# Kernel tuning notes

Hardware: AMD Instinct MI355X
Metric: run time of the kernel (lower is better)

Reference implementation:

```python
import jax, jax.numpy as jnp
import numpy as np

M = 8      # num_modules
H = 128    # hidden_size per module
IN = 512   # input_size
MH = M * H

def _block_mask():
    # mask[mi*H:(mi+1)*H, mi*H:] = 1 (module mi reads modules >= mi)
    m = np.zeros((MH, MH), dtype=np.float32)
    for mi in range(M):
        m[mi*H:(mi+1)*H, mi*H:] = 1.0
    return jnp.asarray(m)

def _active_sizes(T):
    # number of active modules at step t: t=0 -> M, else min(M, trailing_zeros(t)+1)
    sizes = []
    for t in range(T):
        ma = 0
        while t % (2 ** ma) == 0 and ma < M:
            ma += 1
        sizes.append(ma * H)
    return jnp.asarray(np.array(sizes, dtype=np.int32))

def setup_inputs() -> dict:
    key = jax.random.key(0)
    k1, k2, k3, k4 = jax.random.split(key, 4)
    T, B = 256, 128
    scale = 1.0 / np.sqrt(MH)
    x = jax.random.normal(k1, (T, B, IN), dtype=jnp.float32)
    h_prev = jnp.zeros((B, MH), dtype=jnp.float32)
    Wxh = jax.random.normal(k2, (MH, IN), dtype=jnp.float32) * scale
    Whh = jax.random.normal(k3, (MH, MH), dtype=jnp.float32) * scale
    bh = jax.random.normal(k4, (MH,), dtype=jnp.float32) * scale
    return {"x": x, "h_prev": h_prev, "Wxh": Wxh, "Whh": Whh, "bh": bh}

def reference(x, h_prev, Wxh, Whh, bh):
    T = x.shape[0]
    mask = _block_mask()
    Whh_m = Whh * mask  # clockwork block-triangular mask, reapplied as in torch
    thresholds = _active_sizes(T)          # [T] active hidden width per step
    idx = jnp.arange(MH)

    # Precompute input projections for all timesteps: [T, B, MH]
    xW = jnp.einsum('tbi,hi->tbh', x, Wxh)

    def step(h, inp):
        xw_t, thr = inp
        # full-width update; rows < thr equal the torch sliced-matmul result
        h_full = h @ Whh_m.T + xw_t + bh
        h_new = jnp.where(idx < thr, h_full, h)
        return h_new, h_new

    h_last, out = jax.lax.scan(step, h_prev, (xW, thresholds))
    return (out, h_last)
```

## Files before the change

kernel.cpp:

```cpp
#include <hip/hip_runtime.h>
#include <hip/hip_bf16.h>


#define TT 256
#define BB 128
#define INW 512
#define HH 128
#define MHW 1024

typedef __bf16 bf16x8 __attribute__((ext_vector_type(8)));
typedef __bf16 bf16x4 __attribute__((ext_vector_type(4)));
typedef float f32x4 __attribute__((ext_vector_type(4)));

__constant__ unsigned int c_hmod_off[8] = {
    0u, 4194304u, 6291456u, 7340032u, 7864320u, 8126464u, 8257536u, 8323072u};

__device__ __forceinline__ int active_thr(int t) {
    int ma = (t == 0) ? 8 : min(__ffs(t), 8);
    return ma * HH;
}

__device__ __forceinline__ unsigned short f2bf(float f) {
    union { float f; unsigned int u; } v{f};
    unsigned int r = v.u + 0x7FFFu + ((v.u >> 16) & 1u);
    return (unsigned short)(r >> 16);
}
__device__ __forceinline__ unsigned int pack2(float lo, float hi) {
    return (unsigned int)f2bf(lo) | ((unsigned int)f2bf(hi) << 16);
}
__device__ __forceinline__ float bf2f(unsigned short u) {
    union { unsigned int i; float f; } v;
    v.i = ((unsigned int)u) << 16;
    return v.f;
}

__device__ __forceinline__ void gld_lds16(const void* g, char* l) {
    __builtin_amdgcn_global_load_lds(
        (const __attribute__((address_space(1))) void*)g,
        (__attribute__((address_space(3))) void*)l, 16, 0, 0);
}

__device__ __forceinline__ bf16x8 frag_ld(const char* tile, int row, int ks, int lane) {
    int off = (row * 128 + ks * 64 + (lane >> 4) * 16) ^ ((row & 7) << 4);
    return *reinterpret_cast<const bf16x8*>(tile + off);
}

__device__ __forceinline__ bf16x8 frag_ld_f32(const char* tile, int row, int ks, int g) {
    int off = ((row << 8) + ks * 128 + g * 32) ^ ((row & 7) << 4);
    f32x4 a = *reinterpret_cast<const f32x4*>(tile + off);
    f32x4 b = *reinterpret_cast<const f32x4*>(tile + (off ^ 16));
    bf16x8 u;
    u[0] = (__bf16)a[0]; u[1] = (__bf16)a[1]; u[2] = (__bf16)a[2]; u[3] = (__bf16)a[3];
    u[4] = (__bf16)b[0]; u[5] = (__bf16)b[1]; u[6] = (__bf16)b[2]; u[7] = (__bf16)b[3];
    return u;
}

__global__ __launch_bounds__(256) void k_xw(const float* __restrict__ x,
                                            const float* __restrict__ Wxh,
                                            const float* __restrict__ bh,
                                            float* __restrict__ xwb) {
    __shared__ char ldsW[2][32768];
    __shared__ char ldsX[2][16384];
    int id = blockIdx.x >> 1, half = blockIdx.x & 1;
    int rt = 0, rem = id;
    while (rem >= (256 >> rt)) { rem -= 256 >> rt; ++rt; }
    int t = rem << rt;

    int tid = threadIdx.x, lane = tid & 63, wid = tid >> 6;
    int l15 = lane & 15, g = lane >> 4;
    int wr = (wid >> 1) * 64, wc = (wid & 1) * 32;

    const float* gW[8];
    const float* gX[4];
    {
        int kb = (lane & 15) * 16;
#pragma unroll
        for (int i = 0; i < 8; ++i) {
            int row = i * 16 + wid * 4 + (lane >> 4);
            int kf = (kb ^ ((row & 7) << 4)) >> 2;
            gW[i] = Wxh + (size_t)(rt * 128 + row) * INW + kf;
        }
#pragma unroll
        for (int i = 0; i < 4; ++i) {
            int row = i * 16 + wid * 4 + (lane >> 4);
            int kf = (kb ^ ((row & 7) << 4)) >> 2;
            gX[i] = x + ((size_t)t * BB + half * 64 + row) * INW + kf;
        }
    }
#pragma unroll
    for (int i = 0; i < 8; ++i)
        gld_lds16(gW[i], &ldsW[0][0] + i * 4096 + wid * 1024);
#pragma unroll
    for (int i = 0; i < 4; ++i)
        gld_lds16(gX[i], &ldsX[0][0] + i * 4096 + wid * 1024);

    f32x4 acc[4][2] = {};
    for (int c = 0; c < 8; ++c) {
        int cur = c & 1;
        __syncthreads();
        if (c < 7) {
#pragma unroll
            for (int i = 0; i < 8; ++i)
                gld_lds16(gW[i] + (c + 1) * 64,
                          &ldsW[cur ^ 1][0] + i * 4096 + wid * 1024);
#pragma unroll
            for (int i = 0; i < 4; ++i)
                gld_lds16(gX[i] + (c + 1) * 64,
                          &ldsX[cur ^ 1][0] + i * 4096 + wid * 1024);
        }
#pragma unroll
        for (int ks = 0; ks < 2; ++ks) {
            bf16x8 fa[4], fb[2];
#pragma unroll
            for (int i = 0; i < 4; ++i)
                fa[i] = frag_ld_f32(&ldsW[cur][0], wr + i * 16 + l15, ks, g);
#pragma unroll
            for (int j = 0; j < 2; ++j)
                fb[j] = frag_ld_f32(&ldsX[cur][0], wc + j * 16 + l15, ks, g);
#pragma unroll
            for (int i = 0; i < 4; ++i)
#pragma unroll
                for (int j = 0; j < 2; ++j)
                    acc[i][j] = __builtin_amdgcn_mfma_f32_16x16x32_bf16(
                        fa[i], fb[j], acc[i][j], 0, 0, 0);
        }
    }
#pragma unroll
    for (int i = 0; i < 4; ++i) {
        int rbase = rt * 128 + wr + i * 16 + g * 4;
        float4 bias = *reinterpret_cast<const float4*>(&bh[rbase]);
#pragma unroll
        for (int j = 0; j < 2; ++j) {
            int b = half * 64 + wc + j * 16 + l15;
            float4 v = make_float4(acc[i][j][0] + bias.x, acc[i][j][1] + bias.y,
                                   acc[i][j][2] + bias.z, acc[i][j][3] + bias.w);
            *reinterpret_cast<float4*>(
                &xwb[(size_t)(t * BB + b) * MHW + rbase]) = v;
        }
    }
}

__global__ __launch_bounds__(256) void k_u(const float* __restrict__ Whh,
                                           const float* __restrict__ hprev,
                                           const unsigned short* __restrict__ hmod,
                                           float* __restrict__ xwb, int mi) {
    __shared__ char lds[131072];
    char* ldsA0 = lds;
    char* ldsA1 = lds + 32768;
    char* ldsH0 = lds + 65536;
    char* ldsH1 = lds + 98304;
    int k = blockIdx.x;
    int t = k << mi;
    int tid = threadIdx.x, lane = tid & 63, wid = tid >> 6;
    int l15 = lane & 15, g = lane >> 4;
    int wr = (wid >> 1) * 64, wc = (wid & 1) * 64;
    int ntile = 2 * (7 - mi);

    const float* gA[8];
    {
        int kb = l15 * 16;
#pragma unroll
        for (int i = 0; i < 8; ++i) {
            int row = i * 16 + wid * 4 + g;
            int kf = (kb ^ ((row & 7) << 4)) >> 2;
            gA[i] = Whh + (size_t)(mi * HH + row) * MHW + kf;
        }
    }
    f32x4 acc[4][4] = {};

    if (k == 0) {
        const float* gH[8];
        {
            int kb = l15 * 16;
#pragma unroll
            for (int i = 0; i < 8; ++i) {
                int row = i * 16 + wid * 4 + g;
                int kf = (kb ^ ((row & 7) << 4)) >> 2;
                gH[i] = hprev + (size_t)row * MHW + kf;
            }
        }
        auto stage = [&](int tt, char* dA, char* dH) {
            int j = mi + 1 + (tt >> 1), c0 = (tt & 1) * 64;
            int off = j * HH + c0;
#pragma unroll
            for (int i = 0; i < 8; ++i)
                gld_lds16(gA[i] + off, dA + i * 4096 + wid * 1024);
#pragma unroll
            for (int i = 0; i < 8; ++i)
                gld_lds16(gH[i] + off, dH + i * 4096 + wid * 1024);
        };
        stage(0, ldsA0, ldsH0);
        for (int tt = 0; tt < ntile; ++tt) {
            int cur = tt & 1;
            __syncthreads();
            if (tt + 1 < ntile)
                stage(tt + 1, cur ? ldsA0 : ldsA1, cur ? ldsH0 : ldsH1);
            const char* sA = cur ? ldsA1 : ldsA0;
            const char* sH = cur ? ldsH1 : ldsH0;
#pragma unroll
            for (int ks = 0; ks < 2; ++ks) {
                bf16x8 fa[4], fb[4];
#pragma unroll
                for (int i = 0; i < 4; ++i) {
                    fa[i] = frag_ld_f32(sA, wr + i * 16 + l15, ks, g);
                    fb[i] = frag_ld_f32(sH, wc + i * 16 + l15, ks, g);
                }
#pragma unroll
                for (int i = 0; i < 4; ++i)
#pragma unroll
                    for (int jj = 0; jj < 4; ++jj)
                        acc[i][jj] = __builtin_amdgcn_mfma_f32_16x16x32_bf16(
                            fa[i], fb[jj], acc[i][jj], 0, 0, 0);
            }
        }
    } else {
        size_t hoff[4];
        {
            int cb = ((lane & 7) * 16) ^ ((lane >> 3) << 4);
#pragma unroll
            for (int p = 0; p < 4; ++p) {
                int row = p * 32 + wid * 8 + (lane >> 3);
                hoff[p] = (size_t)row * HH + (cb >> 1);
            }
        }
        auto stage = [&](int tt, char* dA, char* dH) {
            int j = mi + 1 + (tt >> 1), c0 = (tt & 1) * 64;
            int offA = j * HH + c0;
#pragma unroll
            for (int i = 0; i < 8; ++i)
                gld_lds16(gA[i] + offA, dA + i * 4096 + wid * 1024);
            const unsigned short* hb =
                hmod + c_hmod_off[j] + (size_t)((t - 1) >> j) * BB * HH + c0;
#pragma unroll
            for (int p = 0; p < 4; ++p)
                gld_lds16(hb + hoff[p], dH + p * 4096 + wid * 1024);
        };
        stage(0, ldsA0, ldsH0);
        for (int tt = 0; tt < ntile; ++tt) {
            int cur = tt & 1;
            __syncthreads();
            if (tt + 1 < ntile)
                stage(tt + 1, cur ? ldsA0 : ldsA1, cur ? ldsH0 : ldsH1);
            const char* sA = cur ? ldsA1 : ldsA0;
            const char* sH = cur ? ldsH1 : ldsH0;
#pragma unroll
            for (int ks = 0; ks < 2; ++ks) {
                bf16x8 fa[4], fb[4];
#pragma unroll
                for (int i = 0; i < 4; ++i) {
                    fa[i] = frag_ld_f32(sA, wr + i * 16 + l15, ks, g);
                    fb[i] = frag_ld(sH, wc + i * 16 + l15, ks, lane);
                }
#pragma unroll
                for (int i = 0; i < 4; ++i)
#pragma unroll
                    for (int jj = 0; jj < 4; ++jj)
                        acc[i][jj] = __builtin_amdgcn_mfma_f32_16x16x32_bf16(
                            fa[i], fb[jj], acc[i][jj], 0, 0, 0);
            }
        }
    }
#pragma unroll
    for (int i = 0; i < 4; ++i) {
        int rbase = wr + i * 16 + g * 4;
#pragma unroll
        for (int j = 0; j < 4; ++j) {
            int b = wc + j * 16 + l15;
            float4* p = reinterpret_cast<float4*>(
                &xwb[(size_t)(t * BB + b) * MHW + mi * HH + rbase]);
            float4 v = *p;
            v.x += acc[i][j][0]; v.y += acc[i][j][1];
            v.z += acc[i][j][2]; v.w += acc[i][j][3];
            *p = v;
        }
    }
}

#define SYNC_LDS()                                              \
    do {                                                        \
        asm volatile("s_waitcnt lgkmcnt(0)" ::: "memory");      \
        __builtin_amdgcn_sched_barrier(0);                      \
        __builtin_amdgcn_s_barrier();                           \
        __builtin_amdgcn_sched_barrier(0);                      \
    } while (0)
#define SYNC_VM24()                                             \
    do {                                                        \
        asm volatile("s_waitcnt vmcnt(24)" ::: "memory");       \
        __builtin_amdgcn_sched_barrier(0);                      \
        __builtin_amdgcn_s_barrier();                           \
        __builtin_amdgcn_sched_barrier(0);                      \
    } while (0)

__global__ __launch_bounds__(256) void k_phase(const float* __restrict__ Whh,
                                               const float* __restrict__ hprev,
                                               const float* __restrict__ xwb,
                                               unsigned short* __restrict__ hmod,
                                               int mi) {
    int b0 = blockIdx.x * 16;
    int tid = threadIdx.x, lane = tid & 63, wid = tid >> 6;
    int l15 = lane & 15, g = lane >> 4;
    __shared__ char sH[2][4096];
    __shared__ char sU[8][8192];
    int Tm = TT >> mi;

    if (wid < 2) {
        bf16x8 Af[4][4];
        {
            const float* Ab = Whh + (size_t)(mi * HH) * MHW + mi * HH;
#pragma unroll
            for (int mm = 0; mm < 4; ++mm) {
                const float* row = Ab + (size_t)(64 * wid + mm * 16 + l15) * MHW;
#pragma unroll
                for (int kf = 0; kf < 4; ++kf) {
                    float4 v0 = *reinterpret_cast<const float4*>(row + kf * 32 + g * 8);
                    float4 v1 = *reinterpret_cast<const float4*>(row + kf * 32 + g * 8 + 4);
                    bf16x8 u;
                    u[0] = (__bf16)v0.x; u[1] = (__bf16)v0.y;
                    u[2] = (__bf16)v0.z; u[3] = (__bf16)v0.w;
                    u[4] = (__bf16)v1.x; u[5] = (__bf16)v1.y;
                    u[6] = (__bf16)v1.z; u[7] = (__bf16)v1.w;
                    Af[mm][kf] = u;
                }
            }
        }
#pragma unroll
        for (int p = 0; p < 2; ++p) {
            int tt = tid + p * 128;
            int b = tt >> 4, r8 = (tt & 15) * 8;
            const float* hp = hprev + (size_t)(b0 + b) * MHW + mi * HH + r8;
            float4 v0 = *reinterpret_cast<const float4*>(hp);
            float4 v1 = *reinterpret_cast<const float4*>(hp + 4);
            uint4 pk;
            pk.x = pack2(v0.x, v0.y); pk.y = pack2(v0.z, v0.w);
            pk.z = pack2(v1.x, v1.y); pk.w = pack2(v1.z, v1.w);
            int off = (b * 256 + r8 * 2) ^ ((b & 7) << 4);
            *reinterpret_cast<uint4*>(&sH[0][0] + off) = pk;
        }
        int roff[4], woff[4], uoff[4];
#pragma unroll
        for (int kf = 0; kf < 4; ++kf)
            roff[kf] = (l15 * 256 + kf * 64 + g * 16) ^ ((l15 & 7) << 4);
#pragma unroll
        for (int mm = 0; mm < 4; ++mm) {
            woff[mm] = (l15 * 256 + (64 * wid + mm * 16 + g * 4) * 2) ^ ((l15 & 7) << 4);
            uoff[mm] = (16 * wid + 4 * mm + g) * 256 + l15 * 16;
        }
        SYNC_LDS();

        for (int K = 0; K < Tm; ++K) {
            int cur = K & 1;
            const char* ub = &sU[K & 7][0];
            f32x4 acc[4], acc2[4];
#pragma unroll
            for (int mm = 0; mm < 4; ++mm) {
                acc[mm] = *reinterpret_cast<const f32x4*>(ub + uoff[mm]);
                acc2[mm] = (f32x4){0.f, 0.f, 0.f, 0.f};
            }
            bf16x8 Bf[4];
#pragma unroll
            for (int kf = 0; kf < 4; ++kf)
                Bf[kf] = *reinterpret_cast<const bf16x8*>(&sH[cur][0] + roff[kf]);
#pragma unroll
            for (int mm = 0; mm < 4; ++mm) {
                acc[mm] = __builtin_amdgcn_mfma_f32_16x16x32_bf16(
                    Af[mm][0], Bf[0], acc[mm], 0, 0, 0);
                acc2[mm] = __builtin_amdgcn_mfma_f32_16x16x32_bf16(
                    Af[mm][2], Bf[2], acc2[mm], 0, 0, 0);
                acc[mm] = __builtin_amdgcn_mfma_f32_16x16x32_bf16(
                    Af[mm][1], Bf[1], acc[mm], 0, 0, 0);
                acc2[mm] = __builtin_amdgcn_mfma_f32_16x16x32_bf16(
                    Af[mm][3], Bf[3], acc2[mm], 0, 0, 0);
            }
#pragma unroll
            for (int mm = 0; mm < 4; ++mm) {
                acc[mm] += acc2[mm];
                bf16x4 pk;
                pk[0] = (__bf16)acc[mm][0]; pk[1] = (__bf16)acc[mm][1];
                pk[2] = (__bf16)acc[mm][2]; pk[3] = (__bf16)acc[mm][3];
                *reinterpret_cast<bf16x4*>(&sH[cur ^ 1][0] + woff[mm]) = pk;
            }
            SYNC_LDS();
        }
    } else if (wid == 2) {
        const float* ubase = xwb + (size_t)(b0 + l15) * MHW + mi * HH + g * 4;
#pragma unroll
        for (int q = 0; q < 4; ++q) {
            int t = min(q, Tm - 1) << mi;
            const float* pt = ubase + (size_t)t * BB * MHW;
#pragma unroll
            for (int p = 0; p < 8; ++p)
                gld_lds16(pt + p * 16, &sU[q][0] + p * 1024);
        }
        SYNC_VM24();
        for (int K = 0; K < Tm; ++K) {
            int t = min(K + 4, Tm - 1) << mi;
            int slot = (K + 4) & 7;
            const float* pt = ubase + (size_t)t * BB * MHW;
#pragma unroll
            for (int p = 0; p < 8; ++p)
                gld_lds16(pt + p * 16, &sU[slot][0] + p * 1024);
            SYNC_VM24();
        }
        asm volatile("s_waitcnt vmcnt(0)" ::: "memory");
    } else {
        int bq = lane >> 2;
        int rr = (lane & 3) * 32;
        unsigned short* hm =
            hmod + c_hmod_off[mi] + (size_t)(b0 + bq) * HH + rr;
        int soff[4];
#pragma unroll
        for (int c = 0; c < 4; ++c)
            soff[c] = (bq * 256 + (rr + c * 8) * 2) ^ ((bq & 7) << 4);
        SYNC_LDS();
        for (int K = 0; K < Tm; ++K) {
            if (K >= 1) {
                uint4 h[4];
#pragma unroll
                for (int c = 0; c < 4; ++c)
                    h[c] = *reinterpret_cast<const uint4*>(&sH[K & 1][0] + soff[c]);
                unsigned short* dst = hm + (size_t)(K - 1) * BB * HH;
#pragma unroll
                for (int c = 0; c < 4; ++c)
                    *reinterpret_cast<uint4*>(dst + c * 8) = h[c];
            }
            SYNC_LDS();
        }
        {
            uint4 h[4];
#pragma unroll
            for (int c = 0; c < 4; ++c)
                h[c] = *reinterpret_cast<const uint4*>(&sH[Tm & 1][0] + soff[c]);
            unsigned short* dst = hm + (size_t)(Tm - 1) * BB * HH;
#pragma unroll
            for (int c = 0; c < 4; ++c)
                *reinterpret_cast<uint4*>(dst + c * 8) = h[c];
        }
    }
}

__global__ __launch_bounds__(256) void k_out(const unsigned short* __restrict__ hmod,
                                             float* __restrict__ out) {
    int b = blockIdx.x, t = blockIdx.y;
    int tid = threadIdx.x;
    int i = tid * 4;
    int j = i >> 7;
    int k = t >> j;
    ushort4 h = *reinterpret_cast<const ushort4*>(
        &hmod[c_hmod_off[j] + ((size_t)k * BB + b) * HH + (i & 127)]);
    float4 v = make_float4(bf2f(h.x), bf2f(h.y), bf2f(h.z), bf2f(h.w));
    *reinterpret_cast<float4*>(&out[((size_t)t * BB + b) * MHW + i]) = v;
    if (t == TT - 1) {
        *reinterpret_cast<float4*>(
            &out[(size_t)TT * BB * MHW + (size_t)b * MHW + i]) = v;
    }
}

extern "C" void kernel_launch(void* const* d_in, const int* in_sizes, int n_in,
                              void* d_out, int out_size, void* d_ws, size_t ws_size,
                              hipStream_t stream) {
    const float* x = (const float*)d_in[0];
    const float* hprev = (const float*)d_in[1];
    const float* Wxh = (const float*)d_in[2];
    const float* Whh = (const float*)d_in[3];
    const float* bh = (const float*)d_in[4];
    float* out = (float*)d_out;

    float* xwb = out;
    unsigned short* hmod = (unsigned short*)d_ws;

    k_xw<<<dim3(1020), 256, 0, stream>>>(x, Wxh, bh, xwb);

    for (int mi = 7; mi >= 0; --mi) {
        if (mi < 7)
            k_u<<<dim3(TT >> mi), 256, 0, stream>>>(Whh, hprev, hmod, xwb, mi);
        k_phase<<<8, 256, 0, stream>>>(Whh, hprev, xwb, hmod, mi);
    }

    k_out<<<dim3(128, 256), 256, 0, stream>>>(hmod, out);
}
```

Measured before the change: 404.1 us.

## Parallelize serial recurrence for fast modules via matrix-power chunked scan

For modules 0 and 1 (the longest sequential chains), the recurrence is split into chunks of 8 steps. Powers of the diagonal Whh block are precomputed (k_pow), and in-chunk partial sums are built in parallel (k_s). Only chunk boundaries run serially, using the 8th power (k_comb), and the intermediate states are then expanded in parallel (k_exp). This shortens the serial dependency chain by about 8x in exchange for extra matmul work and more kernel launches. Repeated bf16 rounding of the matrix powers may also add numerical error.

```diff
diff --git a/kernel.cpp b/kernel.cpp
--- a/kernel.cpp
+++ b/kernel.cpp
@@ -15,11 +15,6 @@
 __constant__ unsigned int c_hmod_off[8] = {
     0u, 4194304u, 6291456u, 7340032u, 7864320u, 8126464u, 8257536u, 8323072u};
 
-__device__ __forceinline__ int active_thr(int t) {
-    int ma = (t == 0) ? 8 : min(__ffs(t), 8);
-    return ma * HH;
-}
-
 __device__ __forceinline__ unsigned short f2bf(float f) {
     union { float f; unsigned int u; } v{f};
     unsigned int r = v.u + 0x7FFFu + ((v.u >> 16) & 1u);
@@ -40,11 +35,33 @@
         (__attribute__((address_space(3))) void*)l, 16, 0, 0);
 }
 
+__device__ __forceinline__ void stage_load(float4 (&v)[8],
+                                           const float* __restrict__ src,
+                                           int stride, int tid) {
+    int k4 = (tid & 15) * 4;
+    int r0 = tid >> 4;
+#pragma unroll
+    for (int p = 0; p < 8; ++p)
+        v[p] = *reinterpret_cast<const float4*>(src + (size_t)(p * 16 + r0) * stride + k4);
+}
+__device__ __forceinline__ void stage_write(char* dst, const float4 (&v)[8], int tid) {
+    int k8 = (tid & 15) * 8;
+    int r0 = tid >> 4;
+#pragma unroll
+    for (int p = 0; p < 8; ++p) {
+        int row = p * 16 + r0;
+        ushort4 b;
+        b.x = f2bf(v[p].x); b.y = f2bf(v[p].y);
+        b.z = f2bf(v[p].z); b.w = f2bf(v[p].w);
+        int off = (row * 128 + k8) ^ ((row & 7) << 4);
+        *reinterpret_cast<ushort4*>(dst + off) = b;
+    }
+}
+
 __device__ __forceinline__ bf16x8 frag_ld(const char* tile, int row, int ks, int lane) {
     int off = (row * 128 + ks * 64 + (lane >> 4) * 16) ^ ((row & 7) << 4);
     return *reinterpret_cast<const bf16x8*>(tile + off);
 }
-
 __device__ __forceinline__ bf16x8 frag_ld_f32(const char* tile, int row, int ks, int g) {
     int off = ((row << 8) + ks * 128 + g * 32) ^ ((row & 7) << 4);
     f32x4 a = *reinterpret_cast<const f32x4*>(tile + off);
@@ -53,6 +70,26 @@
     u[0] = (__bf16)a[0]; u[1] = (__bf16)a[1]; u[2] = (__bf16)a[2]; u[3] = (__bf16)a[3];
     u[4] = (__bf16)b[0]; u[5] = (__bf16)b[1]; u[6] = (__bf16)b[2]; u[7] = (__bf16)b[3];
     return u;
+}
+
+__device__ __forceinline__ void mfma_tile(const char* sA, const char* sB,
+                                          f32x4 (&acc)[4][4], int lane,
+                                          int wr, int wc) {
+#pragma unroll
+    for (int ks = 0; ks < 2; ++ks) {
+        bf16x8 fa[4], fb[4];
+#pragma unroll
+        for (int i = 0; i < 4; ++i) {
+            fa[i] = frag_ld(sA, wr + i * 16 + (lane & 15), ks, lane);
+            fb[i] = frag_ld(sB, wc + i * 16 + (lane & 15), ks, lane);
+        }
+#pragma unroll
+        for (int i = 0; i < 4; ++i)
+#pragma unroll
+            for (int j = 0; j < 4; ++j)
+                acc[i][j] = __builtin_amdgcn_mfma_f32_16x16x32_bf16(
+                    fa[i], fb[j], acc[i][j], 0, 0, 0);
+    }
 }
 
 __global__ __launch_bounds__(256) void k_xw(const float* __restrict__ x,
@@ -137,6 +174,70 @@
             *reinterpret_cast<float4*>(
                 &xwb[(size_t)(t * BB + b) * MHW + rbase]) = v;
         }
+    }
+}
+
+__global__ __launch_bounds__(256) void k_pow(const float* __restrict__ Whh,
+                                             float* __restrict__ P) {
+    int mi = blockIdx.x;
+    __shared__ char X[2][16384];
+    __shared__ char Bt[2][16384];
+    int tid = threadIdx.x, lane = tid & 63, wid = tid >> 6;
+    int l15 = lane & 15, g = lane >> 4;
+    int wr = (wid >> 1) * 64, wc = (wid & 1) * 64;
+    const float* Ab = Whh + (size_t)(mi * HH) * MHW + mi * HH;
+    float* Pm = P + (size_t)mi * 8 * 16384;
+
+#pragma unroll
+    for (int ck = 0; ck < 2; ++ck) {
+        float4 vA[8];
+        stage_load(vA, Ab + ck * 64, MHW, tid);
+        stage_write(&X[ck][0], vA, tid);
+        int k4 = (tid & 15) * 4;
+        int r0 = tid >> 4;
+#pragma unroll
+        for (int p = 0; p < 8; ++p) {
+            int row = p * 16 + r0;
+            ushort4 b;
+            b.x = f2bf(Ab[(size_t)(ck * 64 + k4 + 0) * MHW + row]);
+            b.y = f2bf(Ab[(size_t)(ck * 64 + k4 + 1) * MHW + row]);
+            b.z = f2bf(Ab[(size_t)(ck * 64 + k4 + 2) * MHW + row]);
+            b.w = f2bf(Ab[(size_t)(ck * 64 + k4 + 3) * MHW + row]);
+            int off = (row * 128 + k4 * 2) ^ ((row & 7) << 4);
+            *reinterpret_cast<ushort4*>(&Bt[ck][0] + off) = b;
+        }
+    }
+    for (int idx = tid * 4; idx < 16384; idx += 1024) {
+        int r = idx >> 7, cq = idx & 127;
+        *reinterpret_cast<float4*>(&Pm[idx]) =
+            *reinterpret_cast<const float4*>(&Ab[(size_t)r * MHW + cq]);
+    }
+    __syncthreads();
+
+    for (int q = 1; q < 8; ++q) {
+        f32x4 acc[4][4] = {};
+        mfma_tile(&X[0][0], &Bt[0][0], acc, lane, wr, wc);
+        mfma_tile(&X[1][0], &Bt[1][0], acc, lane, wr, wc);
+        __syncthreads();
+        float* Pq = Pm + (size_t)q * 16384;
+#pragma unroll
+        for (int i = 0; i < 4; ++i) {
+            int r0 = wr + i * 16 + g * 4;
+#pragma unroll
+            for (int jq = 0; jq < 4; ++jq) {
+                int c = wc + jq * 16 + l15;
+#pragma unroll
+                for (int rr = 0; rr < 4; ++rr) {
+                    float v = acc[i][jq][rr];
+                    Pq[(size_t)(r0 + rr) * 128 + c] = v;
+                    int ck = c >> 6;
+                    int off = (((r0 + rr) * 128) + (c & 63) * 2) ^
+                              (((r0 + rr) & 7) << 4);
+                    *reinterpret_cast<__bf16*>(&X[ck][0] + off) = (__bf16)v;
+                }
+            }
+        }
+        __syncthreads();
     }
 }
 
@@ -276,6 +377,87 @@
     }
 }
 
+__global__ __launch_bounds__(256) void k_s(const float* __restrict__ P,
+                                           float* __restrict__ xwb, int mi) {
+    __shared__ char lds[131072];
+    char* ldsA0 = lds;
+    char* ldsA1 = lds + 32768;
+    char* ldsH0 = lds + 65536;
+    char* ldsH1 = lds + 98304;
+    int c = blockIdx.x, i = blockIdx.y;
+    int tid = threadIdx.x, lane = tid & 63, wid = tid >> 6;
+    int l15 = lane & 15, g = lane >> 4;
+    int wr = (wid >> 1) * 64, wc = (wid & 1) * 64;
+    int mcol = mi * HH, scol = (mi + 1) * HH;
+    int ntile = 2 * i;
+    f32x4 acc[4][4] = {};
+
+    if (ntile > 0) {
+        const float* gA[8];
+        const float* gH[8];
+        {
+            int kb = l15 * 16;
+#pragma unroll
+            for (int i_ = 0; i_ < 8; ++i_) {
+                int row = i_ * 16 + wid * 4 + g;
+                int kf = (kb ^ ((row & 7) << 4)) >> 2;
+                gA[i_] = P + (size_t)row * 128 + kf;
+                gH[i_] = xwb + (size_t)row * MHW + mcol + kf;
+            }
+        }
+        auto stage = [&](int tt, char* dA, char* dH) {
+            int p = tt >> 1, c0 = (tt & 1) * 64;
+            size_t offA = (size_t)(mi * 8 + (i - 1 - p)) * 16384 + c0;
+            size_t offH = (size_t)((8 * c + p) << mi) * BB * MHW + c0;
+#pragma unroll
+            for (int i_ = 0; i_ < 8; ++i_)
+                gld_lds16(gA[i_] + offA, dA + i_ * 4096 + wid * 1024);
+#pragma unroll
+            for (int i_ = 0; i_ < 8; ++i_)
+                gld_lds16(gH[i_] + offH, dH + i_ * 4096 + wid * 1024);
+        };
+        stage(0, ldsA0, ldsH0);
+        for (int tt = 0; tt < ntile; ++tt) {
+            int cur = tt & 1;
+            __syncthreads();
+            if (tt + 1 < ntile)
+                stage(tt + 1, cur ? ldsA0 : ldsA1, cur ? ldsH0 : ldsH1);
+            const char* sA = cur ? ldsA1 : ldsA0;
+            const char* sH = cur ? ldsH1 : ldsH0;
+#pragma unroll
+            for (int ks = 0; ks < 2; ++ks) {
+                bf16x8 fa[4], fb[4];
+#pragma unroll
+                for (int i_ = 0; i_ < 4; ++i_) {
+                    fa[i_] = frag_ld_f32(sA, wr + i_ * 16 + l15, ks, g);
+                    fb[i_] = frag_ld_f32(sH, wc + i_ * 16 + l15, ks, g);
+                }
+#pragma unroll
+                for (int i_ = 0; i_ < 4; ++i_)
+#pragma unroll
+                    for (int jj = 0; jj < 4; ++jj)
+                        acc[i_][jj] = __builtin_amdgcn_mfma_f32_16x16x32_bf16(
+                            fa[i_], fb[jj], acc[i_][jj], 0, 0, 0);
+            }
+        }
+    }
+    int tI = (8 * c + i) << mi;
+#pragma unroll
+    for (int i_ = 0; i_ < 4; ++i_) {
+        int rbase = wr + i_ * 16 + g * 4;
+#pragma unroll
+        for (int j = 0; j < 4; ++j) {
+            int b = wc + j * 16 + l15;
+            float4 u4 = *reinterpret_cast<const float4*>(
+                &xwb[(size_t)(tI * BB + b) * MHW + mcol + rbase]);
+            float4 v = make_float4(acc[i_][j][0] + u4.x, acc[i_][j][1] + u4.y,
+                                   acc[i_][j][2] + u4.z, acc[i_][j][3] + u4.w);
+            *reinterpret_cast<float4*>(
+                &xwb[(size_t)(tI * BB + b) * MHW + scol + rbase]) = v;
+        }
+    }
+}
+
 #define SYNC_LDS()                                              \
     do {                                                        \
         asm volatile("s_waitcnt lgkmcnt(0)" ::: "memory");      \
@@ -291,6 +473,268 @@
         __builtin_amdgcn_sched_barrier(0);                      \
     } while (0)
 
+__global__ __launch_bounds__(256) void k_comb(const float* __restrict__ P,
+                                              const float* __restrict__ hprev,
+                                              const float* __restrict__ xwb,
+                                              unsigned short* __restrict__ hmod,
+                                              int mi) {
+    int b0 = blockIdx.x * 16;
+    int tid = threadIdx.x, lane = tid & 63, wid = tid >> 6;
+    int l15 = lane & 15, g = lane >> 4;
+    __shared__ char sH[2][4096];
+    __shared__ char sU[8][8192];
+    int C = (TT >> mi) >> 3;
+    int scol = (mi + 1) * HH;
+    const float* P8 = P + (size_t)(mi * 8 + 7) * 16384;
+
+    if (wid < 2) {
+        bf16x8 Af[4][4];
+        {
+#pragma unroll
+            for (int mm = 0; mm < 4; ++mm) {
+                const float* row = P8 + (size_t)(64 * wid + mm * 16 + l15) * 128;
+#pragma unroll
+                for (int kf = 0; kf < 4; ++kf) {
+                    float4 v0 = *reinterpret_cast<const float4*>(row + kf * 32 + g * 8);
+                    float4 v1 = *reinterpret_cast<const float4*>(row + kf * 32 + g * 8 + 4);
+                    bf16x8 u;
+                    u[0] = (__bf16)v0.x; u[1] = (__bf16)v0.y;
+                    u[2] = (__bf16)v0.z; u[3] = (__bf16)v0.w;
+                    u[4] = (__bf16)v1.x; u[5] = (__bf16)v1.y;
+                    u[6] = (__bf16)v1.z; u[7] = (__bf16)v1.w;
+                    Af[mm][kf] = u;
+                }
+            }
+        }
+#pragma unroll
+        for (int p = 0; p < 2; ++p) {
+            int tt = tid + p * 128;
+            int b = tt >> 4, r8 = (tt & 15) * 8;
+            const float* hp = hprev + (size_t)(b0 + b) * MHW + mi * HH + r8;
+            float4 v0 = *reinterpret_cast<const float4*>(hp);
+            float4 v1 = *reinterpret_cast<const float4*>(hp + 4);
+            uint4 pk;
+            pk.x = pack2(v0.x, v0.y); pk.y = pack2(v0.z, v0.w);
+            pk.z = pack2(v1.x, v1.y); pk.w = pack2(v1.z, v1.w);
+            int off = (b * 256 + r8 * 2) ^ ((b & 7) << 4);
+            *reinterpret_cast<uint4*>(&sH[0][0] + off) = pk;
+        }
+        int roff[4], woff[4], uoff[4];
+#pragma unroll
+        for (int kf = 0; kf < 4; ++kf)
+            roff[kf] = (l15 * 256 + kf * 64 + g * 16) ^ ((l15 & 7) << 4);
+#pragma unroll
+        for (int mm = 0; mm < 4; ++mm) {
+            woff[mm] = (l15 * 256 + (64 * wid + mm * 16 + g * 4) * 2) ^ ((l15 & 7) << 4);
+            uoff[mm] = (16 * wid + 4 * mm + g) * 256 + l15 * 16;
+        }
+        SYNC_LDS();
+
+        for (int K = 0; K < C; ++K) {
+            int cur = K & 1;
+            const char* ub = &sU[K & 7][0];
+            f32x4 acc[4], acc2[4];
+#pragma unroll
+            for (int mm = 0; mm < 4; ++mm) {
+                acc[mm] = *reinterpret_cast<const f32x4*>(ub + uoff[mm]);
+                acc2[mm] = (f32x4){0.f, 0.f, 0.f, 0.f};
+            }
+            bf16x8 Bf[4];
+#pragma unroll
+            for (int kf = 0; kf < 4; ++kf)
+                Bf[kf] = *reinterpret_cast<const bf16x8*>(&sH[cur][0] + roff[kf]);
+#pragma unroll
+            for (int mm = 0; mm < 4; ++mm) {
+                acc[mm] = __builtin_amdgcn_mfma_f32_16x16x32_bf16(
+                    Af[mm][0], Bf[0], acc[mm], 0, 0, 0);
+                acc2[mm] = __builtin_amdgcn_mfma_f32_16x16x32_bf16(
+                    Af[mm][2], Bf[2], acc2[mm], 0, 0, 0);
+                acc[mm] = __builtin_amdgcn_mfma_f32_16x16x32_bf16(
+                    Af[mm][1], Bf[1], acc[mm], 0, 0, 0);
+                acc2[mm] = __builtin_amdgcn_mfma_f32_16x16x32_bf16(
+                    Af[mm][3], Bf[3], acc2[mm], 0, 0, 0);
+            }
+#pragma unroll
+            for (int mm = 0; mm < 4; ++mm) {
+                acc[mm] += acc2[mm];
+                bf16x4 pk;
+                pk[0] = (__bf16)acc[mm][0]; pk[1] = (__bf16)acc[mm][1];
+                pk[2] = (__bf16)acc[mm][2]; pk[3] = (__bf16)acc[mm][3];
+                *reinterpret_cast<bf16x4*>(&sH[cur ^ 1][0] + woff[mm]) = pk;
+            }
+            SYNC_LDS();
+        }
+    } else if (wid == 2) {
+        const float* ubase = xwb + (size_t)(b0 + l15) * MHW + scol + g * 4;
+#pragma unroll
+        for (int q = 0; q < 4; ++q) {
+            int t = (8 * min(q, C - 1) + 7) << mi;
+            const float* pt = ubase + (size_t)t * BB * MHW;
+#pragma unroll
+            for (int p = 0; p < 8; ++p)
+                gld_lds16(pt + p * 16, &sU[q][0] + p * 1024);
+        }
+        SYNC_VM24();
+        for (int K = 0; K < C; ++K) {
+            int t = (8 * min(K + 4, C - 1) + 7) << mi;
+            int slot = (K + 4) & 7;
+            const float* pt = ubase + (size_t)t * BB * MHW;
+#pragma unroll
+            for (int p = 0; p < 8; ++p)
+                gld_lds16(pt + p * 16, &sU[slot][0] + p * 1024);
+            SYNC_VM24();
+        }
+        asm volatile("s_waitcnt vmcnt(0)" ::: "memory");
+    } else {
+        int bq = lane >> 2;
+        int rr = (lane & 3) * 32;
+        unsigned short* hm =
+            hmod + c_hmod_off[mi] + (size_t)(b0 + bq) * HH + rr;
+        int soff[4];
+#pragma unroll
+        for (int c = 0; c < 4; ++c)
+            soff[c] = (bq * 256 + (rr + c * 8) * 2) ^ ((bq & 7) << 4);
+        SYNC_LDS();
+        for (int K = 0; K < C; ++K) {
+            if (K >= 1) {
+                uint4 h[4];
+#pragma unroll
+                for (int c = 0; c < 4; ++c)
+                    h[c] = *reinterpret_cast<const uint4*>(&sH[K & 1][0] + soff[c]);
+                unsigned short* dst = hm + (size_t)(8 * (K - 1) + 7) * BB * HH;
+#pragma unroll
+                for (int c = 0; c < 4; ++c)
+                    *reinterpret_cast<uint4*>(dst + c * 8) = h[c];
+            }
+            SYNC_LDS();
+        }
+        {
+            uint4 h[4];
+#pragma unroll
+            for (int c = 0; c < 4; ++c)
+                h[c] = *reinterpret_cast<const uint4*>(&sH[C & 1][0] + soff[c]);
+            unsigned short* dst = hm + (size_t)(8 * (C - 1) + 7) * BB * HH;
+#pragma unroll
+            for (int c = 0; c < 4; ++c)
+                *reinterpret_cast<uint4*>(dst + c * 8) = h[c];
+        }
+    }
+}
+
+__global__ __launch_bounds__(256) void k_exp(const float* __restrict__ P,
+                                             const float* __restrict__ hprev,
+                                             const float* __restrict__ xwb,
+                                             unsigned short* __restrict__ hmod,
+                                             int mi) {
+    __shared__ char lds[131072];
+    char* sB = lds;
+    char* sA = lds + 65536;
+    int c = blockIdx.x;
+    int tid = threadIdx.x, lane = tid & 63, wid = tid >> 6;
+    int l15 = lane & 15, g = lane >> 4;
+    int wr = (wid >> 1) * 64, wc = (wid & 1) * 64;
+    int scol = (mi + 1) * HH;
+    bool bndf32 = (c == 0);
+
+    if (bndf32) {
+        const float* gH[8];
+        {
+            int kb = l15 * 16;
+#pragma unroll
+            for (int i_ = 0; i_ < 8; ++i_) {
+                int row = i_ * 16 + wid * 4 + g;
+                int kf = (kb ^ ((row & 7) << 4)) >> 2;
+                gH[i_] = hprev + (size_t)row * MHW + mi * HH + kf;
+            }
+        }
+#pragma unroll
+        for (int ck = 0; ck < 2; ++ck)
+#pragma unroll
+            for (int i_ = 0; i_ < 8; ++i_)
+                gld_lds16(gH[i_] + ck * 64, sB + ck * 32768 + i_ * 4096 + wid * 1024);
+    } else {
+        size_t hoff[4];
+        {
+            int cb = ((lane & 7) * 16) ^ ((lane >> 3) << 4);
+#pragma unroll
+            for (int p = 0; p < 4; ++p) {
+                int row = p * 32 + wid * 8 + (lane >> 3);
+                hoff[p] = (size_t)row * HH + (cb >> 1);
+            }
+        }
+        const unsigned short* hb =
+            hmod + c_hmod_off[mi] + (size_t)(8 * (c - 1) + 7) * BB * HH;
+#pragma unroll
+        for (int ck = 0; ck < 2; ++ck)
+#pragma unroll
+            for (int p = 0; p < 4; ++p)
+                gld_lds16(hb + ck * 64 + hoff[p],
+                          sB + ck * 16384 + p * 4096 + wid * 1024);
+    }
+    const float* gA[8];
+    {
+        int kb = l15 * 16;
+#pragma unroll
+        for (int i_ = 0; i_ < 8; ++i_) {
+            int row = i_ * 16 + wid * 4 + g;
+            int kf = (kb ^ ((row & 7) << 4)) >> 2;
+            gA[i_] = P + (size_t)row * 128 + kf;
+        }
+    }
+
+    for (int i = 0; i < 7; ++i) {
+        __syncthreads();
+        {
+            size_t offA = (size_t)(mi * 8 + i) * 16384;
+#pragma unroll
+            for (int ck = 0; ck < 2; ++ck)
+#pragma unroll
+                for (int i_ = 0; i_ < 8; ++i_)
+                    gld_lds16(gA[i_] + offA + ck * 64,
+                              sA + ck * 32768 + i_ * 4096 + wid * 1024);
+        }
+        __syncthreads();
+        f32x4 acc[4][4] = {};
+#pragma unroll
+        for (int ck = 0; ck < 2; ++ck) {
+#pragma unroll
+            for (int ks = 0; ks < 2; ++ks) {
+                bf16x8 fa[4], fb[4];
+#pragma unroll
+                for (int i_ = 0; i_ < 4; ++i_) {
+                    fa[i_] = frag_ld_f32(sA + ck * 32768, wr + i_ * 16 + l15, ks, g);
+                    fb[i_] = bndf32
+                        ? frag_ld_f32(sB + ck * 32768, wc + i_ * 16 + l15, ks, g)
+                        : frag_ld(sB + ck * 16384, wc + i_ * 16 + l15, ks, lane);
+                }
+#pragma unroll
+                for (int i_ = 0; i_ < 4; ++i_)
+#pragma unroll
+                    for (int jj = 0; jj < 4; ++jj)
+                        acc[i_][jj] = __builtin_amdgcn_mfma_f32_16x16x32_bf16(
+                            fa[i_], fb[jj], acc[i_][jj], 0, 0, 0);
+            }
+        }
+        int tI = (8 * c + i) << mi;
+#pragma unroll
+        for (int i_ = 0; i_ < 4; ++i_) {
+            int rbase = wr + i_ * 16 + g * 4;
+#pragma unroll
+            for (int j = 0; j < 4; ++j) {
+                int b = wc + j * 16 + l15;
+                float4 s4 = *reinterpret_cast<const float4*>(
+                    &xwb[(size_t)(tI * BB + b) * MHW + scol + rbase]);
+                uint2 pk;
+                pk.x = pack2(acc[i_][j][0] + s4.x, acc[i_][j][1] + s4.y);
+                pk.y = pack2(acc[i_][j][2] + s4.z, acc[i_][j][3] + s4.w);
+                *reinterpret_cast<uint2*>(
+                    &hmod[c_hmod_off[mi] + ((size_t)(8 * c + i) * BB + b) * HH +
+                          rbase]) = pk;
+            }
+        }
+    }
+}
+
 __global__ __launch_bounds__(256) void k_phase(const float* __restrict__ Whh,
                                                const float* __restrict__ hprev,
                                                const float* __restrict__ xwb,
@@ -467,14 +911,23 @@
 
     float* xwb = out;
     unsigned short* hmod = (unsigned short*)d_ws;
+    float* P = (float*)((char*)d_ws + 16711680);
 
     k_xw<<<dim3(1020), 256, 0, stream>>>(x, Wxh, bh, xwb);
-
-    for (int mi = 7; mi >= 0; --mi) {
+    k_pow<<<dim3(2), 256, 0, stream>>>(Whh, P);
+
+    for (int mi = 7; mi >= 2; --mi) {
         if (mi < 7)
             k_u<<<dim3(TT >> mi), 256, 0, stream>>>(Whh, hprev, hmod, xwb, mi);
         k_phase<<<8, 256, 0, stream>>>(Whh, hprev, xwb, hmod, mi);
     }
+    for (int mi = 1; mi >= 0; --mi) {
+        int C = (TT >> mi) >> 3;
+        k_u<<<dim3(TT >> mi), 256, 0, stream>>>(Whh, hprev, hmod, xwb, mi);
+        k_s<<<dim3(C, 8), 256, 0, stream>>>(P, xwb, mi);
+        k_comb<<<8, 256, 0, stream>>>(P, hprev, xwb, hmod, mi);
+        k_exp<<<dim3(C), 256, 0, stream>>>(P, hprev, xwb, hmod, mi);
+    }
 
     k_out<<<dim3(128, 256), 256, 0, stream>>>(hmod, out);
 }
```

After: 438.8 us. 8.6% more time.
